# Kernel optimization log

Hardware: AMD Instinct MI355X
Metric: run time of the kernel (lower is better)

Reference implementation:

```python
import jax, jax.numpy as jnp
import numpy as np

N, D_IN, D_OUT, E, K, H = 8192, 256, 256, 16, 2, 512


def setup_inputs() -> dict:
    key = jax.random.key(0)
    ks = jax.random.split(key, 11)
    return {
        "x": jax.random.normal(ks[0], (N, D_IN), jnp.float32),
        "gate_w": jax.random.normal(ks[1], (D_IN, H), jnp.float32),
        "gate_b": jax.random.normal(ks[2], (H,), jnp.float32),
        "gate_out_w": jax.random.normal(ks[3], (H, E), jnp.float32),
        "gate_out_b": jax.random.normal(ks[4], (E,), jnp.float32),
        "mlp_w1": jax.random.normal(ks[5], (D_IN, E, H), jnp.float32),
        "mlp_b1": jax.random.normal(ks[6], (E, H), jnp.float32),
        "mlp_w2": jax.random.normal(ks[7], (H, E, H), jnp.float32),
        "mlp_b2": jax.random.normal(ks[8], (E, H), jnp.float32),
        "mlp_w3": jax.random.normal(ks[9], (H, E, D_OUT), jnp.float32),
        "mlp_b3": jax.random.normal(ks[10], (E, D_OUT), jnp.float32),
    }


def reference(x, gate_w, gate_b, gate_out_w, gate_out_b,
              mlp_w1, mlp_b1, mlp_w2, mlp_b2, mlp_w3, mlp_b3):
    n, e = x.shape[0], gate_out_w.shape[1]
    # Gate MLP: relu(x @ Wg + bg) @ Wo + bo -> [N, E]
    logits = jax.nn.relu(x @ gate_w + gate_b) @ gate_out_w + gate_out_b
    # Top-k expert selection + softmax over selected gate values
    top_vals, top_idx = jax.lax.top_k(logits, K)              # [N, K]
    gates = jax.nn.softmax(top_vals, axis=-1)                 # [N, K]
    # Scatter into a sparse combine matrix [N, E] (top-k indices are unique per row)
    combine = jnp.zeros((n, e), x.dtype).at[jnp.arange(n)[:, None], top_idx].set(gates)
    # Per-expert 3-layer MLP, computed densely over all experts then combined.
    h1 = jax.nn.relu(jnp.einsum('ni,ieh->neh', x, mlp_w1) + mlp_b1)    # [N, E, H]
    h2 = jax.nn.relu(jnp.einsum('neh,heg->neg', h1, mlp_w2) + mlp_b2)  # [N, E, H]
    ye = jnp.einsum('neg,geo->neo', h2, mlp_w3) + mlp_b3               # [N, E, D_OUT]
    # Gate-weighted combine over experts (only top-k contribute)
    return jnp.einsum('neo,ne->no', ye, combine)
```

## Files before the change

kernel.cpp:

```cpp
#include <hip/hip_runtime.h>
#include <hip/hip_bf16.h>
#include <stdint.h>

#define NTOK 8192
#define DIN  256
#define DOUT 256
#define NEXP 16
#define HID  512
#define NKA  (NTOK*2)
#define NBLK (NTOK/256)
#define MAXTILE 272
#define GK 768

typedef __bf16 bf16x8 __attribute__((ext_vector_type(8)));
typedef __bf16 bf16x4 __attribute__((ext_vector_type(4)));
typedef float  f32x4  __attribute__((ext_vector_type(4)));

__device__ __forceinline__ void async_cp16(const __bf16* g, __bf16* l) {
  __builtin_amdgcn_global_load_lds(
      (const __attribute__((address_space(1))) unsigned int*)g,
      (__attribute__((address_space(3))) unsigned int*)l, 16, 0, 0);
}

__device__ __forceinline__ void transpose_cvt_body(const float* __restrict__ src,
                                                   __bf16* __restrict__ dst,
                                                   int K, int N, int bx, int by, int bz,
                                                   int tx, int ty, float (*t)[33]) {
  int e = bz, k0 = bx * 32, n0 = by * 32;
  #pragma unroll
  for (int j = 0; j < 4; j++) {
    int kl = ty + j * 8;
    t[kl][tx] = src[(size_t)(k0 + kl) * (NEXP * N) + (size_t)e * N + n0 + tx];
  }
  __syncthreads();
  #pragma unroll
  for (int j = 0; j < 4; j++) {
    int nl = ty + j * 8;
    dst[(size_t)e * N * K + (size_t)(n0 + nl) * K + k0 + tx] = (__bf16)t[tx][nl];
  }
}

__global__ __launch_bounds__(256) void prep_kernel(
    const float* __restrict__ x, __bf16* __restrict__ xs,
    const float* __restrict__ gw, __bf16* __restrict__ gwt,
    float* __restrict__ logitz) {
  __shared__ float t[32][33];
  int idx = blockIdx.x;
  int tid = threadIdx.x;
  int tx = tid & 31, ty = tid >> 5;
  if (idx < 2048) {
    int i = idx * 256 + tid;
    float4 v = ((const float4*)x)[i];
    int base = i * 4;
    int tk = base >> 8, c = base & 255;
    bf16x4 hi = { (__bf16)v.x, (__bf16)v.y, (__bf16)v.z, (__bf16)v.w };
    bf16x4 lo = { (__bf16)(v.x - (float)hi[0]), (__bf16)(v.y - (float)hi[1]),
                  (__bf16)(v.z - (float)hi[2]), (__bf16)(v.w - (float)hi[3]) };
    __bf16* row = xs + (size_t)tk * GK + c;
    *(bf16x4*)(row)       = hi;
    *(bf16x4*)(row + 256) = lo;
    *(bf16x4*)(row + 512) = hi;
  } else if (idx < 2176) {
    int g = idx - 2048;
    int k0 = (g & 7) * 32, n0 = (g >> 3) * 32;
    #pragma unroll
    for (int j = 0; j < 4; j++) {
      int kl = ty + j * 8;
      t[kl][tx] = gw[(size_t)(k0 + kl) * HID + n0 + tx];
    }
    __syncthreads();
    #pragma unroll
    for (int j = 0; j < 4; j++) {
      int nl = ty + j * 8;
      float v = t[tx][nl];
      __bf16 hi = (__bf16)v;
      __bf16 lo = (__bf16)(v - (float)hi);
      __bf16* drow = gwt + (size_t)(n0 + nl) * GK + k0 + tx;
      drow[0]   = hi;
      drow[256] = hi;
      drow[512] = lo;
    }
  } else {
    int i = (idx - 2176) * 256 + tid;
    ((float4*)logitz)[i] = make_float4(0.f, 0.f, 0.f, 0.f);
  }
}

__global__ __launch_bounds__(256) void gate_fused_kernel(
    const __bf16* __restrict__ xs, const __bf16* __restrict__ gwt,
    const float* __restrict__ gate_b, float* __restrict__ logits,
    const float* __restrict__ gow,
    const float* __restrict__ w1, __bf16* __restrict__ w1t,
    const float* __restrict__ w2, __bf16* __restrict__ w2t,
    const float* __restrict__ w3, __bf16* __restrict__ w3t) {
  __shared__ __align__(16) char smem[49152];
  int bx = blockIdx.x;
  int tid = threadIdx.x;

  if (bx >= 512) {
    float (*t)[33] = (float (*)[33])smem;
    int tx = tid & 31, ty = tid >> 5;
    int g = bx - 512;
    if (g < 2048) {
      transpose_cvt_body(w1, w1t, DIN, HID, g & 7, (g >> 3) & 15, g >> 7, tx, ty, t);
    } else if (g < 6144) {
      int g2 = g - 2048;
      transpose_cvt_body(w2, w2t, HID, HID, g2 & 15, (g2 >> 4) & 15, g2 >> 8, tx, ty, t);
    } else {
      int g3 = g - 6144;
      transpose_cvt_body(w3, w3t, HID, DOUT, g3 & 15, (g3 >> 4) & 7, g3 >> 7, tx, ty, t);
    }
    return;
  }

  int mt = bx >> 2, nt = bx & 3;
  __bf16* AlB = (__bf16*)smem;
  __bf16* BlB = (__bf16*)(smem + 16384);

  int lane = tid & 63, w = tid >> 6;
  int l16 = lane & 15, quad = lane >> 4;

  int r0 = tid >> 3;
  int q8 = ((tid & 7) ^ (r0 & 7)) * 8;
  const __bf16* apg0 = xs + (size_t)(mt * 64 + r0) * GK + q8;
  const __bf16* apg1 = apg0 + (size_t)32 * GK;
  const __bf16* bpg0 = gwt + (size_t)(nt * 128 + r0) * GK + q8;
  const __bf16* bpg1 = bpg0 + (size_t)32 * GK;
  const __bf16* bpg2 = bpg0 + (size_t)64 * GK;
  const __bf16* bpg3 = bpg0 + (size_t)96 * GK;

  __bf16* al0 = AlB;
  __bf16* al1 = AlB + 4096;
  __bf16* bl0 = BlB;
  __bf16* bl1 = BlB + 8192;

  f32x4 acc[4][2];
  #pragma unroll
  for (int i = 0; i < 4; i++)
    #pragma unroll
    for (int j = 0; j < 2; j++) acc[i][j] = {0.f, 0.f, 0.f, 0.f};

  async_cp16(apg0, al0 + tid * 8);
  async_cp16(apg1, al0 + (tid + 256) * 8);
  async_cp16(bpg0, bl0 + tid * 8);
  async_cp16(bpg1, bl0 + (tid + 256) * 8);
  async_cp16(bpg2, bl0 + (tid + 512) * 8);
  async_cp16(bpg3, bl0 + (tid + 768) * 8);

  int x7 = (l16 & 7);

  const int nIter = GK >> 6;
  for (int it = 0; it < nIter; ++it) {
    int buf = it & 1;
    if (it + 1 < nIter) {
      int kb = (it + 1) << 6;
      __bf16* an = buf ? al0 : al1;
      __bf16* bn = buf ? bl0 : bl1;
      async_cp16(apg0 + kb, an + tid * 8);
      async_cp16(apg1 + kb, an + (tid + 256) * 8);
      async_cp16(bpg0 + kb, bn + tid * 8);
      async_cp16(bpg1 + kb, bn + (tid + 256) * 8);
      async_cp16(bpg2 + kb, bn + (tid + 512) * 8);
      async_cp16(bpg3 + kb, bn + (tid + 768) * 8);
      asm volatile("s_waitcnt vmcnt(6)" ::: "memory");
    } else {
      asm volatile("s_waitcnt vmcnt(0)" ::: "memory");
    }
    __builtin_amdgcn_s_barrier();
    asm volatile("" ::: "memory");
    const __bf16* ab = buf ? al1 : al0;
    const __bf16* bb = buf ? bl1 : bl0;
    #pragma unroll
    for (int kk = 0; kk < 2; kk++) {
      int qs = ((kk * 4 + quad) ^ x7) * 8;
      bf16x8 af[4], bfr[2];
      #pragma unroll
      for (int i = 0; i < 4; i++)
        af[i] = *(const bf16x8*)(ab + (size_t)(i * 16 + l16) * 64 + qs);
      #pragma unroll
      for (int i = 0; i < 2; i++)
        bfr[i] = *(const bf16x8*)(bb + (size_t)(w * 32 + i * 16 + l16) * 64 + qs);
      #pragma unroll
      for (int mi = 0; mi < 4; mi++)
        #pragma unroll
        for (int ni = 0; ni < 2; ni++)
          acc[mi][ni] = __builtin_amdgcn_mfma_f32_16x16x32_bf16(af[mi], bfr[ni], acc[mi][ni], 0, 0, 0);
    }
    asm volatile("" ::: "memory");
    __builtin_amdgcn_s_barrier();
  }

  __syncthreads();
  float* wl = (float*)smem;
  float* ht = (float*)(smem + 8192);
  if (tid < 128) {
    const float* gr = gow + (size_t)(nt * 128 + tid) * 16;
    #pragma unroll
    for (int j = 0; j < 4; j++)
      *(float4*)&wl[tid * 16 + j * 4] = *(const float4*)&gr[j * 4];
  }
  float bv[2];
  #pragma unroll
  for (int ni = 0; ni < 2; ni++) bv[ni] = gate_b[nt * 128 + w * 32 + ni * 16 + l16];
  #pragma unroll
  for (int mi = 0; mi < 4; mi++)
    #pragma unroll
    for (int ni = 0; ni < 2; ni++)
      #pragma unroll
      for (int r = 0; r < 4; r++) {
        int row = mi * 16 + quad * 4 + r;
        int col = w * 32 + ni * 16 + l16;
        ht[row * 132 + col] = fmaxf(acc[mi][ni][r] + bv[ni], 0.f);
      }
  __syncthreads();
  int t = tid >> 2, e4 = (tid & 3) * 4;
  float s0 = 0.f, s1 = 0.f, s2 = 0.f, s3 = 0.f;
  #pragma unroll 4
  for (int h = 0; h < 128; h++) {
    float hv = ht[t * 132 + h];
    const float* wr = &wl[h * 16 + e4];
    s0 = fmaf(hv, wr[0], s0);
    s1 = fmaf(hv, wr[1], s1);
    s2 = fmaf(hv, wr[2], s2);
    s3 = fmaf(hv, wr[3], s3);
  }
  float* lp = logits + (size_t)(mt * 64 + t) * 16 + e4;
  atomicAdd(lp + 0, s0);
  atomicAdd(lp + 1, s1);
  atomicAdd(lp + 2, s2);
  atomicAdd(lp + 3, s3);
}

__global__ __launch_bounds__(256) void top2_kernel(const float* __restrict__ logits,
                                                   const float* __restrict__ gb,
                                                   int2* __restrict__ e01,
                                                   float2* __restrict__ g01,
                                                   int* __restrict__ lrank,
                                                   int* __restrict__ blockhist) {
  __shared__ int hist[NEXP];
  __shared__ float gbl[NEXP];
  int tid = threadIdx.x;
  if (tid < NEXP) { hist[tid] = 0; gbl[tid] = gb[tid]; }
  __syncthreads();
  int t = blockIdx.x * 256 + tid;
  float lv[16];
  const float4* lp = (const float4*)(logits + (size_t)t * 16);
  #pragma unroll
  for (int j = 0; j < 4; j++) {
    float4 v = lp[j];
    lv[4*j]   = v.x + gbl[4*j];
    lv[4*j+1] = v.y + gbl[4*j+1];
    lv[4*j+2] = v.z + gbl[4*j+2];
    lv[4*j+3] = v.w + gbl[4*j+3];
  }
  float v0 = -3.402823466e38f, v1 = -3.402823466e38f;
  int i0 = 0, i1 = 0;
  #pragma unroll
  for (int e = 0; e < 16; e++) {
    float v = lv[e];
    if (v > v0) { v1 = v0; i1 = i0; v0 = v; i0 = e; }
    else if (v > v1) { v1 = v; i1 = e; }
  }
  float ew = expf(v1 - v0);
  float inv = 1.f / (1.f + ew);
  e01[t] = make_int2(i0, i1);
  g01[t] = make_float2(inv, ew * inv);
  int r0 = atomicAdd(&hist[i0], 1);
  int r1 = atomicAdd(&hist[i1], 1);
  lrank[2 * t]     = r0;
  lrank[2 * t + 1] = r1;
  __syncthreads();
  if (tid < NEXP) blockhist[blockIdx.x * NEXP + tid] = hist[tid];
}

__global__ __launch_bounds__(256) void fillscan_kernel(const int2* __restrict__ e01,
                                                       const int* __restrict__ lrank,
                                                       const int* __restrict__ blockhist,
                                                       int* __restrict__ tok_sorted,
                                                       int* __restrict__ route_pos,
                                                       int* __restrict__ offsets,
                                                       int* __restrict__ tile_e,
                                                       int* __restrict__ tile_mt,
                                                       int* __restrict__ ntiles) {
  __shared__ int tot_s[NEXP], pre_s[NEXP], soff[NEXP + 1], base_l[NEXP], tbase[NEXP];
  int b = blockIdx.x;
  int tid = threadIdx.x;
  if (tid < NEXP) {
    int s_all = 0, s_pre = 0;
    for (int bb = 0; bb < NBLK; bb++) {
      int h = blockhist[bb * NEXP + tid];
      s_pre += (bb < b) ? h : 0;
      s_all += h;
    }
    tot_s[tid] = s_all;
    pre_s[tid] = s_pre;
  }
  __syncthreads();
  if (tid == 0) {
    int s = 0, tb = 0;
    for (int i = 0; i < NEXP; i++) {
      soff[i] = s; s += tot_s[i];
      tbase[i] = tb; tb += (tot_s[i] + 63) >> 6;
    }
    soff[NEXP] = s;
    if (b == 0) *ntiles = tb;
  }
  __syncthreads();
  if (tid < NEXP) base_l[tid] = soff[tid] + pre_s[tid];
  if (b == 0) {
    if (tid < NEXP + 1) offsets[tid] = soff[tid];
    if (tid < NEXP) {
      int nt = (tot_s[tid] + 63) >> 6, tb0 = tbase[tid];
      for (int m = 0; m < nt; m++) { tile_e[tb0 + m] = tid; tile_mt[tb0 + m] = m; }
    }
  }
  __syncthreads();
  int t = b * 256 + tid;
  int2 e = e01[t];
  int p0 = base_l[e.x] + lrank[2 * t];
  int p1 = base_l[e.y] + lrank[2 * t + 1];
  tok_sorted[p0] = t; route_pos[2 * t]     = p0;
  tok_sorted[p1] = t; route_pos[2 * t + 1] = p1;
}

template<bool RELU>
__global__ __launch_bounds__(256) void moe_gemm_kernel(const __bf16* __restrict__ A,
                                                       const __bf16* __restrict__ Bt,
                                                       const float* __restrict__ bias,
                                                       __bf16* __restrict__ out,
                                                       const int* __restrict__ seg_off,
                                                       const int* __restrict__ gather,
                                                       const int* __restrict__ tile_e,
                                                       const int* __restrict__ tile_mt,
                                                       const int* __restrict__ ntiles,
                                                       int LDA, int K, int N) {
  int bx0 = blockIdx.x;
  int bx = (bx0 & 7) * (MAXTILE >> 3) + (bx0 >> 3);
  if (bx >= *ntiles) return;
  int e  = tile_e[bx];
  int mt = tile_mt[bx];
  int off = seg_off[e];
  int Te  = seg_off[e + 1] - off;
  int nt = blockIdx.y;

  __shared__ __align__(16) char smem[49152];
  __bf16* AlB = (__bf16*)smem;
  __bf16* BlB = (__bf16*)(smem + 16384);

  int tid = threadIdx.x;
  int lane = tid & 63, w = tid >> 6;
  int l16 = lane & 15, quad = lane >> 4;

  int r0 = tid >> 3;
  int q8 = ((tid & 7) ^ (r0 & 7)) * 8;
  int rowA0 = mt * 64 + r0;
  int rowA1 = rowA0 + 32;
  int rA0 = rowA0 < Te ? rowA0 : Te - 1;
  int rA1 = rowA1 < Te ? rowA1 : Te - 1;
  size_t ga0 = gather ? (size_t)gather[off + rA0] : (size_t)(off + rA0);
  size_t ga1 = gather ? (size_t)gather[off + rA1] : (size_t)(off + rA1);
  const __bf16* apg0 = A + ga0 * LDA + q8;
  const __bf16* apg1 = A + ga1 * LDA + q8;
  const __bf16* Bte  = Bt + (size_t)e * N * K;
  const __bf16* bpg0 = Bte + (size_t)(nt * 128 + r0) * K + q8;
  const __bf16* bpg1 = bpg0 + (size_t)32 * K;
  const __bf16* bpg2 = bpg0 + (size_t)64 * K;
  const __bf16* bpg3 = bpg0 + (size_t)96 * K;

  __bf16* al0 = AlB;
  __bf16* al1 = AlB + 4096;
  __bf16* bl0 = BlB;
  __bf16* bl1 = BlB + 8192;

  f32x4 acc[4][2];
  #pragma unroll
  for (int i = 0; i < 4; i++)
    #pragma unroll
    for (int j = 0; j < 2; j++) acc[i][j] = {0.f, 0.f, 0.f, 0.f};

  async_cp16(apg0, al0 + tid * 8);
  async_cp16(apg1, al0 + (tid + 256) * 8);
  async_cp16(bpg0, bl0 + tid * 8);
  async_cp16(bpg1, bl0 + (tid + 256) * 8);
  async_cp16(bpg2, bl0 + (tid + 512) * 8);
  async_cp16(bpg3, bl0 + (tid + 768) * 8);

  int x7 = (l16 & 7);

  int nIter = K >> 6;
  for (int it = 0; it < nIter; ++it) {
    int buf = it & 1;
    if (it + 1 < nIter) {
      int kb = (it + 1) << 6;
      __bf16* an = buf ? al0 : al1;
      __bf16* bn = buf ? bl0 : bl1;
      async_cp16(apg0 + kb, an + tid * 8);
      async_cp16(apg1 + kb, an + (tid + 256) * 8);
      async_cp16(bpg0 + kb, bn + tid * 8);
      async_cp16(bpg1 + kb, bn + (tid + 256) * 8);
      async_cp16(bpg2 + kb, bn + (tid + 512) * 8);
      async_cp16(bpg3 + kb, bn + (tid + 768) * 8);
      asm volatile("s_waitcnt vmcnt(6)" ::: "memory");
    } else {
      asm volatile("s_waitcnt vmcnt(0)" ::: "memory");
    }
    __builtin_amdgcn_s_barrier();
    asm volatile("" ::: "memory");
    const __bf16* ab = buf ? al1 : al0;
    const __bf16* bb = buf ? bl1 : bl0;
    #pragma unroll
    for (int kk = 0; kk < 2; kk++) {
      int qs = ((kk * 4 + quad) ^ x7) * 8;
      bf16x8 af[4], bfr[2];
      #pragma unroll
      for (int i = 0; i < 4; i++)
        af[i] = *(const bf16x8*)(ab + (size_t)(i * 16 + l16) * 64 + qs);
      #pragma unroll
      for (int i = 0; i < 2; i++)
        bfr[i] = *(const bf16x8*)(bb + (size_t)(w * 32 + i * 16 + l16) * 64 + qs);
      #pragma unroll
      for (int mi = 0; mi < 4; mi++)
        #pragma unroll
        for (int ni = 0; ni < 2; ni++)
          acc[mi][ni] = __builtin_amdgcn_mfma_f32_16x16x32_bf16(af[mi], bfr[ni], acc[mi][ni], 0, 0, 0);
    }
    asm volatile("" ::: "memory");
    __builtin_amdgcn_s_barrier();
  }

  const float* be = bias + (size_t)e * N;
  #pragma unroll
  for (int ni = 0; ni < 2; ni++) {
    int col = nt * 128 + w * 32 + ni * 16 + l16;
    float bv = be[col];
    #pragma unroll
    for (int mi = 0; mi < 4; mi++) {
      #pragma unroll
      for (int r = 0; r < 4; r++) {
        int row_in = mt * 64 + mi * 16 + quad * 4 + r;
        if (row_in < Te) {
          float v = acc[mi][ni][r] + bv;
          if (RELU) v = fmaxf(v, 0.f);
          out[(size_t)(off + row_in) * N + col] = (__bf16)v;
        }
      }
    }
  }
}

__global__ void combine_kernel(const __bf16* __restrict__ Y, const int* __restrict__ route_pos,
                               const float2* __restrict__ g01, float* __restrict__ out) {
  int gid = blockIdx.x * blockDim.x + threadIdx.x;
  int t = gid >> 6, c = (gid & 63) << 2;
  if (t >= NTOK) return;
  int p0 = route_pos[2 * t], p1 = route_pos[2 * t + 1];
  float2 g = g01[t];
  bf16x4 y0 = *(const bf16x4*)&Y[(size_t)p0 * DOUT + c];
  bf16x4 y1 = *(const bf16x4*)&Y[(size_t)p1 * DOUT + c];
  float4 o;
  o.x = g.x * (float)y0[0] + g.y * (float)y1[0];
  o.y = g.x * (float)y0[1] + g.y * (float)y1[1];
  o.z = g.x * (float)y0[2] + g.y * (float)y1[2];
  o.w = g.x * (float)y0[3] + g.y * (float)y1[3];
  *(float4*)&out[(size_t)t * DOUT + c] = o;
}

extern "C" void kernel_launch(void* const* d_in, const int* in_sizes, int n_in,
                              void* d_out, int out_size, void* d_ws, size_t ws_size,
                              hipStream_t stream) {
  const float* x          = (const float*)d_in[0];
  const float* gate_w     = (const float*)d_in[1];
  const float* gate_b     = (const float*)d_in[2];
  const float* gate_out_w = (const float*)d_in[3];
  const float* gate_out_b = (const float*)d_in[4];
  const float* w1         = (const float*)d_in[5];
  const float* b1         = (const float*)d_in[6];
  const float* w2         = (const float*)d_in[7];
  const float* b2         = (const float*)d_in[8];
  const float* w3         = (const float*)d_in[9];
  const float* b3         = (const float*)d_in[10];
  float* out = (float*)d_out;

  char* ws = (char*)d_ws;
  size_t o = 0;
  auto alloc = [&](size_t bytes) -> void* {
    o = (o + 255) & ~(size_t)255;
    void* p = ws + o;
    o += bytes;
    return p;
  };

  __bf16* w1t  = (__bf16*)alloc((size_t)NEXP * HID * DIN * 2);
  __bf16* w2t  = (__bf16*)alloc((size_t)NEXP * HID * HID * 2);
  __bf16* w3t  = (__bf16*)alloc((size_t)NEXP * DOUT * HID * 2);
  __bf16* gwt  = (__bf16*)alloc((size_t)HID * GK * 2);
  __bf16* H1   = (__bf16*)alloc((size_t)(NKA + 128) * HID * 2);
  size_t r3 = (size_t)NTOK * GK * 2;
  size_t r4 = (size_t)(NKA + 128) * HID * 2;
  void* region2 = alloc(r3 > r4 ? r3 : r4);
  __bf16* xs = (__bf16*)region2;
  __bf16* H2 = (__bf16*)region2;
  float* logits    = (float*)alloc((size_t)NTOK * 16 * 4);
  int2*  e01       = (int2*)alloc((size_t)NTOK * 8);
  float2* g01      = (float2*)alloc((size_t)NTOK * 8);
  int*   offsets   = (int*)alloc((NEXP + 1) * 4);
  int*   blockhist = (int*)alloc((size_t)NBLK * NEXP * 4);
  int*   lrank     = (int*)alloc((size_t)NTOK * 2 * 4);
  int*   tok_sorted= (int*)alloc((size_t)(NKA + 128) * 4);
  int*   route_pos = (int*)alloc((size_t)NTOK * 2 * 4);
  int*   tile_e    = (int*)alloc(MAXTILE * 4);
  int*   tile_mt   = (int*)alloc(MAXTILE * 4);
  int*   ntiles    = (int*)alloc(4);
  __bf16* Y        = (__bf16*)alloc((size_t)(NKA + 128) * DOUT * 2);
  (void)ws_size; (void)n_in; (void)in_sizes; (void)out_size;

  prep_kernel<<<2304, 256, 0, stream>>>(x, xs, gate_w, gwt, logits);

  gate_fused_kernel<<<8704, 256, 0, stream>>>(xs, gwt, gate_b, logits, gate_out_w,
                                              w1, w1t, w2, w2t, w3, w3t);

  top2_kernel<<<NBLK, 256, 0, stream>>>(logits, gate_out_b, e01, g01, lrank, blockhist);
  fillscan_kernel<<<NBLK, 256, 0, stream>>>(e01, lrank, blockhist, tok_sorted, route_pos,
                                            offsets, tile_e, tile_mt, ntiles);

  moe_gemm_kernel<true><<<dim3(MAXTILE, HID / 128), 256, 0, stream>>>(
      xs, w1t, b1, H1, offsets, tok_sorted, tile_e, tile_mt, ntiles, GK, DIN, HID);
  moe_gemm_kernel<true><<<dim3(MAXTILE, HID / 128), 256, 0, stream>>>(
      H1, w2t, b2, H2, offsets, nullptr, tile_e, tile_mt, ntiles, HID, HID, HID);
  moe_gemm_kernel<false><<<dim3(MAXTILE, DOUT / 128), 256, 0, stream>>>(
      H2, w3t, b3, Y, offsets, nullptr, tile_e, tile_mt, ntiles, HID, HID, DOUT);

  combine_kernel<<<(NTOK * 64) / 256, 256, 0, stream>>>(Y, route_pos, g01, out);
}
```

Before: 190.9 us.

## Fuse top-2 selection and routing scan into one kernel with grid barrier

Merges the top-2 gating kernel and the fill/scan routing kernel into a single launch. The two are joined by a software grid-wide barrier: an atomic counter, reset in the prep kernel, that each block increments and spins on before reading the per-block histograms. Expert indices and ranks stay in registers, so the e01 and lrank intermediate buffers are no longer written and read back. The aim is to save one kernel launch and that global traffic. In exchange it depends on all 32 blocks being resident at the same time, which they are on this GPU, and it adds spin-wait cost.

```diff
diff --git a/kernel.cpp b/kernel.cpp
--- a/kernel.cpp
+++ b/kernel.cpp
@@ -43,7 +43,7 @@
 __global__ __launch_bounds__(256) void prep_kernel(
     const float* __restrict__ x, __bf16* __restrict__ xs,
     const float* __restrict__ gw, __bf16* __restrict__ gwt,
-    float* __restrict__ logitz) {
+    float* __restrict__ logitz, int* __restrict__ counter) {
   __shared__ float t[32][33];
   int idx = blockIdx.x;
   int tid = threadIdx.x;
@@ -81,6 +81,7 @@
       drow[512] = lo;
     }
   } else {
+    if (idx == 2176 && tid == 0) *counter = 0;
     int i = (idx - 2176) * 256 + tid;
     ((float4*)logitz)[i] = make_float4(0.f, 0.f, 0.f, 0.f);
   }
@@ -231,18 +232,26 @@
   atomicAdd(lp + 3, s3);
 }
 
-__global__ __launch_bounds__(256) void top2_kernel(const float* __restrict__ logits,
-                                                   const float* __restrict__ gb,
-                                                   int2* __restrict__ e01,
-                                                   float2* __restrict__ g01,
-                                                   int* __restrict__ lrank,
-                                                   int* __restrict__ blockhist) {
+__global__ __launch_bounds__(256) void route_kernel(const float* __restrict__ logits,
+                                                    const float* __restrict__ gb,
+                                                    float2* __restrict__ g01,
+                                                    int* __restrict__ blockhist,
+                                                    int* __restrict__ counter,
+                                                    int* __restrict__ tok_sorted,
+                                                    int* __restrict__ route_pos,
+                                                    int* __restrict__ offsets,
+                                                    int* __restrict__ tile_e,
+                                                    int* __restrict__ tile_mt,
+                                                    int* __restrict__ ntiles) {
   __shared__ int hist[NEXP];
   __shared__ float gbl[NEXP];
+  __shared__ int tot_s[NEXP], pre_s[NEXP], soff[NEXP + 1], base_l[NEXP], tbase[NEXP];
+  int b = blockIdx.x;
   int tid = threadIdx.x;
   if (tid < NEXP) { hist[tid] = 0; gbl[tid] = gb[tid]; }
   __syncthreads();
-  int t = blockIdx.x * 256 + tid;
+
+  int t = b * 256 + tid;
   float lv[16];
   const float4* lp = (const float4*)(logits + (size_t)t * 16);
   #pragma unroll
@@ -263,32 +272,26 @@
   }
   float ew = expf(v1 - v0);
   float inv = 1.f / (1.f + ew);
-  e01[t] = make_int2(i0, i1);
   g01[t] = make_float2(inv, ew * inv);
   int r0 = atomicAdd(&hist[i0], 1);
   int r1 = atomicAdd(&hist[i1], 1);
-  lrank[2 * t]     = r0;
-  lrank[2 * t + 1] = r1;
-  __syncthreads();
-  if (tid < NEXP) blockhist[blockIdx.x * NEXP + tid] = hist[tid];
-}
-
-__global__ __launch_bounds__(256) void fillscan_kernel(const int2* __restrict__ e01,
-                                                       const int* __restrict__ lrank,
-                                                       const int* __restrict__ blockhist,
-                                                       int* __restrict__ tok_sorted,
-                                                       int* __restrict__ route_pos,
-                                                       int* __restrict__ offsets,
-                                                       int* __restrict__ tile_e,
-                                                       int* __restrict__ tile_mt,
-                                                       int* __restrict__ ntiles) {
-  __shared__ int tot_s[NEXP], pre_s[NEXP], soff[NEXP + 1], base_l[NEXP], tbase[NEXP];
-  int b = blockIdx.x;
-  int tid = threadIdx.x;
+  __syncthreads();
+
+  if (tid < NEXP)
+    __hip_atomic_store(&blockhist[b * NEXP + tid], hist[tid],
+                       __ATOMIC_RELEASE, __HIP_MEMORY_SCOPE_AGENT);
+  __syncthreads();
+  if (tid == 0) {
+    __hip_atomic_fetch_add(counter, 1, __ATOMIC_ACQ_REL, __HIP_MEMORY_SCOPE_AGENT);
+    while (__hip_atomic_load(counter, __ATOMIC_ACQUIRE, __HIP_MEMORY_SCOPE_AGENT) < NBLK) {}
+  }
+  __syncthreads();
+
   if (tid < NEXP) {
     int s_all = 0, s_pre = 0;
     for (int bb = 0; bb < NBLK; bb++) {
-      int h = blockhist[bb * NEXP + tid];
+      int h = __hip_atomic_load(&blockhist[bb * NEXP + tid],
+                                __ATOMIC_ACQUIRE, __HIP_MEMORY_SCOPE_AGENT);
       s_pre += (bb < b) ? h : 0;
       s_all += h;
     }
@@ -315,10 +318,9 @@
     }
   }
   __syncthreads();
-  int t = b * 256 + tid;
-  int2 e = e01[t];
-  int p0 = base_l[e.x] + lrank[2 * t];
-  int p1 = base_l[e.y] + lrank[2 * t + 1];
+
+  int p0 = base_l[i0] + r0;
+  int p1 = base_l[i1] + r1;
   tok_sorted[p0] = t; route_pos[2 * t]     = p0;
   tok_sorted[p1] = t; route_pos[2 * t + 1] = p1;
 }
@@ -501,11 +503,10 @@
   __bf16* xs = (__bf16*)region2;
   __bf16* H2 = (__bf16*)region2;
   float* logits    = (float*)alloc((size_t)NTOK * 16 * 4);
-  int2*  e01       = (int2*)alloc((size_t)NTOK * 8);
   float2* g01      = (float2*)alloc((size_t)NTOK * 8);
   int*   offsets   = (int*)alloc((NEXP + 1) * 4);
   int*   blockhist = (int*)alloc((size_t)NBLK * NEXP * 4);
-  int*   lrank     = (int*)alloc((size_t)NTOK * 2 * 4);
+  int*   counter   = (int*)alloc(4);
   int*   tok_sorted= (int*)alloc((size_t)(NKA + 128) * 4);
   int*   route_pos = (int*)alloc((size_t)NTOK * 2 * 4);
   int*   tile_e    = (int*)alloc(MAXTILE * 4);
@@ -514,14 +515,14 @@
   __bf16* Y        = (__bf16*)alloc((size_t)(NKA + 128) * DOUT * 2);
   (void)ws_size; (void)n_in; (void)in_sizes; (void)out_size;
 
-  prep_kernel<<<2304, 256, 0, stream>>>(x, xs, gate_w, gwt, logits);
+  prep_kernel<<<2304, 256, 0, stream>>>(x, xs, gate_w, gwt, logits, counter);
 
   gate_fused_kernel<<<8704, 256, 0, stream>>>(xs, gwt, gate_b, logits, gate_out_w,
                                               w1, w1t, w2, w2t, w3, w3t);
 
-  top2_kernel<<<NBLK, 256, 0, stream>>>(logits, gate_out_b, e01, g01, lrank, blockhist);
-  fillscan_kernel<<<NBLK, 256, 0, stream>>>(e01, lrank, blockhist, tok_sorted, route_pos,
-                                            offsets, tile_e, tile_mt, ntiles);
+  route_kernel<<<NBLK, 256, 0, stream>>>(logits, gate_out_b, g01, blockhist, counter,
+                                         tok_sorted, route_pos, offsets,
+                                         tile_e, tile_mt, ntiles);
 
   moe_gemm_kernel<true><<<dim3(MAXTILE, HID / 128), 256, 0, stream>>>(
       xs, w1t, b1, H1, offsets, tok_sorted, tile_e, tile_mt, ntiles, GK, DIN, HID);
```

After: 198.4 us. 1.04x slower.
